# Performance work log

Hardware: AMD Instinct MI355X
Metric: run time of the kernel (lower is better)

## Reference

```python
import jax, jax.numpy as jnp
import numpy as np

TEMP = 0.5
EPS = 1e-8  # torch CosineSimilarity eps


def setup_inputs() -> dict:
    key = jax.random.key(0)
    k1, k2 = jax.random.split(key)
    B, D = 4096, 512
    z_i = jax.random.normal(k1, (B, D), dtype=jnp.float32)
    z_j = jax.random.normal(k2, (B, D), dtype=jnp.float32)
    return {"z_i": z_i, "z_j": z_j}


def reference(z_i, z_j):
    B = z_i.shape[0]
    N = 2 * B
    z = jnp.concatenate([z_i, z_j], axis=0)              # [N, D]
    norm = jnp.maximum(jnp.linalg.norm(z, axis=1, keepdims=True), EPS)
    zn = z / norm                                        # unit rows
    sim = jnp.matmul(zn, zn.T) / TEMP                    # [N, N] cosine sims / temperature
    # positives: sim[i, i+B] for i<B and sim[i+B, i] for i<B
    pos = jnp.concatenate([jnp.diagonal(sim, offset=B), jnp.diagonal(sim, offset=-B)])  # [N]
    # CE over logits [pos, negatives] with label 0 == -pos + logsumexp(row without diagonal)
    diag_mask = jnp.eye(N, dtype=bool)
    sim_masked = jnp.where(diag_mask, -jnp.inf, sim)
    lse = jax.nn.logsumexp(sim_masked, axis=1)           # [N]
    loss = jnp.sum(lse - pos) / N                        # CrossEntropyLoss(reduction='sum') / N
    return loss
```

## Files before the change

kernel.cpp:

```cpp
#include <hip/hip_runtime.h>
#include <stdint.h>

#define NROWS 8192
#define HALF_N 4096
#define DIM 512
#define INV_TEMP 2.0f
#define E2SCALE 2.8853900817779268f
#define LN2 0.6931471805599453f
#define NTILES 528
#define NXCD 8
#define TPX (NTILES / NXCD)

typedef int i32x8 __attribute__((ext_vector_type(8)));
typedef float f32x16 __attribute__((ext_vector_type(16)));

__device__ __forceinline__ void gload_lds16(const unsigned char* g, unsigned char* l) {
  __builtin_amdgcn_global_load_lds(
      (const __attribute__((address_space(1))) unsigned int*)(uintptr_t)g,
      (__attribute__((address_space(3))) unsigned int*)(uint32_t)(uintptr_t)l,
      16, 0, 0);
}

__global__ void __launch_bounds__(256) k_normalize(const float* __restrict__ zi,
                                                   const float* __restrict__ zj,
                                                   unsigned char* __restrict__ zn,
                                                   float* __restrict__ sumexp) {
  int tid = threadIdx.x;
  int gid = blockIdx.x * 256 + tid;
  if (gid < NROWS) sumexp[gid] = 0.0f;
  int wave = tid >> 6, lane = tid & 63;
  int row = blockIdx.x * 4 + wave;
  const float* src = (row < HALF_N) ? (zi + (size_t)row * DIM)
                                    : (zj + (size_t)(row - HALF_N) * DIM);
  const float4* s4 = (const float4*)src;
  float4 a = s4[lane];
  float4 b = s4[lane + 64];
  float ss = a.x * a.x + a.y * a.y + a.z * a.z + a.w * a.w +
             b.x * b.x + b.y * b.y + b.z * b.z + b.w * b.w;
#pragma unroll
  for (int off = 32; off > 0; off >>= 1) ss += __shfl_xor(ss, off, 64);
  float inv = 1.0f / fmaxf(sqrtf(ss), 1e-8f);
  int w0 = __builtin_amdgcn_cvt_pk_fp8_f32(a.x * inv, a.y * inv, 0, false);
  w0 = __builtin_amdgcn_cvt_pk_fp8_f32(a.z * inv, a.w * inv, w0, true);
  int w1 = __builtin_amdgcn_cvt_pk_fp8_f32(b.x * inv, b.y * inv, 0, false);
  w1 = __builtin_amdgcn_cvt_pk_fp8_f32(b.z * inv, b.w * inv, w1, true);
  unsigned char* dst = zn + (size_t)row * DIM;
  *((int*)(dst + lane * 4)) = w0;
  *((int*)(dst + 256 + lane * 4)) = w1;
}

__global__ void __launch_bounds__(512, 2) k_simsum(const unsigned char* __restrict__ zn,
                                                   float* __restrict__ sumexp,
                                                   float* __restrict__ posv) {
  __shared__ __align__(16) unsigned char As[3][256 * 64];
  __shared__ __align__(16) unsigned char Bs[3][256 * 64];
  int tid = threadIdx.x;
  int wave = tid >> 6, lane = tid & 63;

  int bswz = (blockIdx.x & (NXCD - 1)) * TPX + (blockIdx.x >> 3);
  int idx = bswz;
  int tn = (int)((sqrtf(8.0f * idx + 1.0f) - 1.0f) * 0.5f);
  while (tn * (tn + 1) / 2 > idx) tn--;
  while ((tn + 1) * (tn + 2) / 2 <= idx) tn++;
  int tm = idx - tn * (tn + 1) / 2;
  int rowBase = tm * 256, colBase = tn * 256;
  int wr = (wave >> 2) * 128, wc = (wave & 3) * 64;
  int h = lane >> 5, c32 = lane & 31;

  int rA = wave * 32 + (lane >> 2);
  int chunk = (lane & 3) ^ ((rA >> 1) & 3);
  const unsigned char* gA = zn + (size_t)(rowBase + rA) * DIM + chunk * 16;
  const unsigned char* gB = zn + (size_t)(colBase + rA) * DIM + chunk * 16;

#define STAGE(b)                                            \
  do {                                                      \
    gload_lds16(gA, &As[b][wave * 2048]);                   \
    gload_lds16(gA + 16 * DIM, &As[b][wave * 2048 + 1024]); \
    gload_lds16(gB, &Bs[b][wave * 2048]);                   \
    gload_lds16(gB + 16 * DIM, &Bs[b][wave * 2048 + 1024]); \
    gA += 64; gB += 64;                                     \
  } while (0)

  f32x16 acc[4][2];
#pragma unroll
  for (int i = 0; i < 4; i++)
#pragma unroll
    for (int j = 0; j < 2; j++)
#pragma unroll
      for (int r = 0; r < 16; r++) acc[i][j][r] = 0.f;

  int sg = (c32 >> 1) & 3;
  int p0 = (2 * h) ^ sg, p1 = p0 ^ 1;
  int aIdx[4] = {(wr + c32) * 4, (wr + 32 + c32) * 4,
                 (wr + 64 + c32) * 4, (wr + 96 + c32) * 4};
  int bIdx[2] = {(wc + c32) * 4, (wc + 32 + c32) * 4};

#define COMPUTE(b)                                                                   \
  do {                                                                               \
    const int4* Av = (const int4*)As[b];                                             \
    const int4* Bv = (const int4*)Bs[b];                                             \
    i32x8 af[4], bfr[2];                                                             \
    _Pragma("unroll") for (int i = 0; i < 4; i++) {                                  \
      int4 lo = Av[aIdx[i] + p0], hi = Av[aIdx[i] + p1];                             \
      af[i] = (i32x8){lo.x, lo.y, lo.z, lo.w, hi.x, hi.y, hi.z, hi.w};               \
    }                                                                                \
    _Pragma("unroll") for (int j = 0; j < 2; j++) {                                  \
      int4 lo = Bv[bIdx[j] + p0], hi = Bv[bIdx[j] + p1];                             \
      bfr[j] = (i32x8){lo.x, lo.y, lo.z, lo.w, hi.x, hi.y, hi.z, hi.w};              \
    }                                                                                \
    __builtin_amdgcn_s_setprio(1);                                                   \
    _Pragma("unroll") for (int i = 0; i < 4; i++)                                    \
      _Pragma("unroll") for (int j = 0; j < 2; j++)                                  \
        acc[i][j] = __builtin_amdgcn_mfma_scale_f32_32x32x64_f8f6f4(                 \
            af[i], bfr[j], acc[i][j], 0, 0,                               \
            0, 0x7F, 0, 0x7F);                                     \
    __builtin_amdgcn_s_setprio(0);                                                   \
  } while (0)

#define ASM_VMCNT(n) asm volatile("s_waitcnt vmcnt(" #n ")" ::: "memory")
#define WINDOW(s, vm)                                        \
  do {                                                       \
    ASM_VMCNT(vm);                                           \
    asm volatile("s_waitcnt lgkmcnt(0)" ::: "memory");       \
    __builtin_amdgcn_sched_barrier(0);                       \
    __builtin_amdgcn_s_barrier();                            \
    __builtin_amdgcn_sched_barrier(0);                       \
    if ((s) + 2 < 8) STAGE(((s) + 2) % 3);                   \
    COMPUTE((s) % 3);                                        \
  } while (0)

  STAGE(0);
  STAGE(1);
  WINDOW(0, 4);
  WINDOW(1, 4);
  WINDOW(2, 4);
  WINDOW(3, 4);
  WINDOW(4, 4);
  WINDOW(5, 4);
  WINDOW(6, 4);
  WINDOW(7, 0);

  bool isDiag = (tm == tn);
  bool hasPos = (tn == tm + 16);
  bool diagLane = (h == ((c32 >> 2) & 1));
  int rsel = (c32 & 3) | ((c32 >> 3) << 2);
  int dj = 2 * (wave & 3) - 4 * (wave >> 2);

  if (diagLane) {
    if (isDiag) {
      if (dj == 0) { acc[0][0][rsel] = -1e30f; acc[1][1][rsel] = -1e30f; }
      else if (dj == 2) { acc[2][0][rsel] = -1e30f; acc[3][1][rsel] = -1e30f; }
    }
    if (hasPos) {
      if (dj == 0) {
        int gr = rowBase + wr + c32;
        float s0 = acc[0][0][rsel] * INV_TEMP, s1 = acc[1][1][rsel] * INV_TEMP;
        posv[gr] = s0; posv[gr + HALF_N] = s0;
        posv[gr + 32] = s1; posv[gr + 32 + HALF_N] = s1;
      } else if (dj == 2) {
        int gr = rowBase + wr + 64 + c32;
        float s0 = acc[2][0][rsel] * INV_TEMP, s1 = acc[3][1][rsel] * INV_TEMP;
        posv[gr] = s0; posv[gr + HALF_N] = s0;
        posv[gr + 32] = s1; posv[gr + 32 + HALF_N] = s1;
      }
    }
  }

  float cp[2] = {0.f, 0.f};
#pragma unroll
  for (int i = 0; i < 4; i++)
#pragma unroll
    for (int r = 0; r < 16; r++) {
      float e0 = __builtin_amdgcn_exp2f(acc[i][0][r] * E2SCALE);
      float e1 = __builtin_amdgcn_exp2f(acc[i][1][r] * E2SCALE);
      cp[0] += e0;
      cp[1] += e1;
      acc[i][0][r] = e0 + e1;
    }

#define FOLD5(RPX)                                                 \
  do {                                                             \
    _Pragma("unroll") for (int t = 0; t < 16; t++) {               \
      float mine = (lane & 16) ? RPX(t + 16) : RPX(t);             \
      float oth = __shfl_xor((lane & 16) ? RPX(t) : RPX(t + 16), 16, 64); \
      RPX(t) = mine + oth;                                         \
    }                                                              \
    _Pragma("unroll") for (int t = 0; t < 8; t++) {                \
      float mine = (lane & 8) ? RPX(t + 8) : RPX(t);               \
      float oth = __shfl_xor((lane & 8) ? RPX(t) : RPX(t + 8), 8, 64); \
      RPX(t) = mine + oth;                                         \
    }                                                              \
    _Pragma("unroll") for (int t = 0; t < 4; t++) {                \
      float mine = (lane & 4) ? RPX(t + 4) : RPX(t);               \
      float oth = __shfl_xor((lane & 4) ? RPX(t) : RPX(t + 4), 4, 64); \
      RPX(t) = mine + oth;                                         \
    }                                                              \
    _Pragma("unroll") for (int t = 0; t < 2; t++) {                \
      float mine = (lane & 2) ? RPX(t + 2) : RPX(t);               \
      float oth = __shfl_xor((lane & 2) ? RPX(t) : RPX(t + 2), 2, 64); \
      RPX(t) = mine + oth;                                         \
    }                                                              \
    {                                                              \
      float mine = (lane & 1) ? RPX(1) : RPX(0);                   \
      float oth = __shfl_xor((lane & 1) ? RPX(0) : RPX(1), 1, 64); \
      RPX(0) = mine + oth;                                         \
    }                                                              \
  } while (0)

#define RPA(t) acc[(t) >> 4][0][(t) & 15]
#define RPB(t) acc[2 + ((t) >> 4)][0][(t) & 15]
  int myrow = rowBase + wr + 32 * (c32 >> 4) + (c32 & 3) + 8 * ((c32 >> 2) & 3) + 4 * h;
  FOLD5(RPA);
  atomicAdd(&sumexp[myrow], RPA(0));
  FOLD5(RPB);
  atomicAdd(&sumexp[myrow + 64], RPB(0));
#undef RPA
#undef RPB

  if (!isDiag) {
    cp[0] += __shfl_xor(cp[0], 32, 64);
    cp[1] += __shfl_xor(cp[1], 32, 64);
    float cv = h ? cp[1] : cp[0];
    atomicAdd(&sumexp[colBase + wc + h * 32 + c32], cv);
  }
#undef STAGE
#undef COMPUTE
#undef WINDOW
#undef ASM_VMCNT
#undef FOLD5
}

__global__ void __launch_bounds__(1024) k_final(const float* __restrict__ sumexp,
                                                const float* __restrict__ posv,
                                                float* __restrict__ out) {
  __shared__ float red[16];
  int tid = threadIdx.x;
  const float4* se4 = (const float4*)sumexp;
  const float4* pv4 = (const float4*)posv;
  float p = 0.f;
#pragma unroll
  for (int c = 0; c < 2; c++) {
    float4 se = se4[tid * 2 + c];
    float4 pv = pv4[tid * 2 + c];
    p += (__builtin_amdgcn_logf(se.x) + __builtin_amdgcn_logf(se.y) +
          __builtin_amdgcn_logf(se.z) + __builtin_amdgcn_logf(se.w)) * LN2 -
         (pv.x + pv.y + pv.z + pv.w);
  }
#pragma unroll
  for (int off = 32; off > 0; off >>= 1) p += __shfl_xor(p, off, 64);
  int wv = tid >> 6, ln = tid & 63;
  if (ln == 0) red[wv] = p;
  __syncthreads();
  if (tid == 0) {
    float t = 0.f;
    for (int w = 0; w < 16; w++) t += red[w];
    out[0] = t / (float)NROWS;
  }
}

extern "C" void kernel_launch(void* const* d_in, const int* in_sizes, int n_in,
                              void* d_out, int out_size, void* d_ws, size_t ws_size,
                              hipStream_t stream) {
  const float* zi = (const float*)d_in[0];
  const float* zj = (const float*)d_in[1];
  unsigned char* zn = (unsigned char*)d_ws;
  float* sumexp = (float*)((char*)d_ws + (size_t)NROWS * DIM);
  float* posv = sumexp + NROWS;
  float* out = (float*)d_out;

  hipLaunchKernelGGL(k_normalize, dim3(2048), dim3(256), 0, stream, zi, zj, zn, sumexp);
  hipLaunchKernelGGL(k_simsum, dim3(NTILES), dim3(512), 0, stream, zn, sumexp, posv);
  hipLaunchKernelGGL(k_final, dim3(1), dim3(1024), 0, stream, sumexp, posv, out);
}
```

Before: 98.09 us.

## Use 256x128 rectangular tiles over the upper triangle with per-element masking

```diff
diff --git a/kernel.cpp b/kernel.cpp
--- a/kernel.cpp
+++ b/kernel.cpp
@@ -7,7 +7,7 @@
 #define INV_TEMP 2.0f
 #define E2SCALE 2.8853900817779268f
 #define LN2 0.6931471805599453f
-#define NTILES 528
+#define NTILES 1056
 #define NXCD 8
 #define TPX (NTILES / NXCD)
 
@@ -49,36 +49,43 @@
   *((int*)(dst + 256 + lane * 4)) = w1;
 }
 
-__global__ void __launch_bounds__(512, 2) k_simsum(const unsigned char* __restrict__ zn,
+__global__ void __launch_bounds__(256, 2) k_simsum(const unsigned char* __restrict__ zn,
                                                    float* __restrict__ sumexp,
                                                    float* __restrict__ posv) {
   __shared__ __align__(16) unsigned char As[3][256 * 64];
-  __shared__ __align__(16) unsigned char Bs[3][256 * 64];
+  __shared__ __align__(16) unsigned char Bs[3][128 * 64];
   int tid = threadIdx.x;
   int wave = tid >> 6, lane = tid & 63;
 
-  int bswz = (blockIdx.x & (NXCD - 1)) * TPX + (blockIdx.x >> 3);
-  int idx = bswz;
-  int tn = (int)((sqrtf(8.0f * idx + 1.0f) - 1.0f) * 0.5f);
-  while (tn * (tn + 1) / 2 > idx) tn--;
-  while ((tn + 1) * (tn + 2) / 2 <= idx) tn++;
-  int tm = idx - tn * (tn + 1) / 2;
-  int rowBase = tm * 256, colBase = tn * 256;
-  int wr = (wave >> 2) * 128, wc = (wave & 3) * 64;
+  int b = blockIdx.x;
+  int idx = (b & (NXCD - 1)) * TPX + (b >> 3);
+  int tm = (int)((65.0f - sqrtf(4225.0f - 4.0f * idx)) * 0.5f);
+  while (tm * (65 - tm) > idx) tm--;
+  while ((tm + 1) * (64 - tm) <= idx) tm++;
+  int tn = idx - tm * (63 - tm);
+  int rowBase = tm * 256, colBase = tn * 128;
+
+  int wr = (wave >> 1) * 128, wc = (wave & 1) * 64;
   int h = lane >> 5, c32 = lane & 31;
 
-  int rA = wave * 32 + (lane >> 2);
-  int chunk = (lane & 3) ^ ((rA >> 1) & 3);
-  const unsigned char* gA = zn + (size_t)(rowBase + rA) * DIM + chunk * 16;
-  const unsigned char* gB = zn + (size_t)(colBase + rA) * DIM + chunk * 16;
-
-#define STAGE(b)                                            \
-  do {                                                      \
-    gload_lds16(gA, &As[b][wave * 2048]);                   \
-    gload_lds16(gA + 16 * DIM, &As[b][wave * 2048 + 1024]); \
-    gload_lds16(gB, &Bs[b][wave * 2048]);                   \
-    gload_lds16(gB + 16 * DIM, &Bs[b][wave * 2048 + 1024]); \
-    gA += 64; gB += 64;                                     \
+  int rA = wave * 64 + (lane >> 2);
+  int cA = (lane & 3) ^ ((rA >> 1) & 3);
+  const unsigned char* gA = zn + (size_t)(rowBase + rA) * DIM + cA * 16;
+  int rB = wave * 32 + (lane >> 2);
+  int cB = (lane & 3) ^ ((rB >> 1) & 3);
+  const unsigned char* gB = zn + (size_t)(colBase + rB) * DIM + cB * 16;
+
+#define STAGE(bf)                                     \
+  do {                                                \
+    unsigned char* la = &As[bf][wave * 4096];         \
+    unsigned char* lb = &Bs[bf][wave * 2048];         \
+    gload_lds16(gA, la);                              \
+    gload_lds16(gA + 16 * DIM, la + 1024);            \
+    gload_lds16(gA + 32 * DIM, la + 2048);            \
+    gload_lds16(gA + 48 * DIM, la + 3072);            \
+    gload_lds16(gB, lb);                              \
+    gload_lds16(gB + 16 * DIM, lb + 1024);            \
+    gA += 64; gB += 64;                               \
   } while (0)
 
   f32x16 acc[4][2];
@@ -95,10 +102,10 @@
                  (wr + 64 + c32) * 4, (wr + 96 + c32) * 4};
   int bIdx[2] = {(wc + c32) * 4, (wc + 32 + c32) * 4};
 
-#define COMPUTE(b)                                                                   \
+#define COMPUTE(bf)                                                                  \
   do {                                                                               \
-    const int4* Av = (const int4*)As[b];                                             \
-    const int4* Bv = (const int4*)Bs[b];                                             \
+    const int4* Av = (const int4*)As[bf];                                            \
+    const int4* Bv = (const int4*)Bs[bf];                                            \
     i32x8 af[4], bfr[2];                                                             \
     _Pragma("unroll") for (int i = 0; i < 4; i++) {                                  \
       int4 lo = Av[aIdx[i] + p0], hi = Av[aIdx[i] + p1];                             \
@@ -131,52 +138,51 @@
 
   STAGE(0);
   STAGE(1);
-  WINDOW(0, 4);
-  WINDOW(1, 4);
-  WINDOW(2, 4);
-  WINDOW(3, 4);
-  WINDOW(4, 4);
-  WINDOW(5, 4);
-  WINDOW(6, 4);
+  WINDOW(0, 6);
+  WINDOW(1, 6);
+  WINDOW(2, 6);
+  WINDOW(3, 6);
+  WINDOW(4, 6);
+  WINDOW(5, 6);
+  WINDOW(6, 6);
   WINDOW(7, 0);
 
-  bool isDiag = (tm == tn);
-  bool hasPos = (tn == tm + 16);
+  int dbase = colBase + wc - rowBase - wr;
+  int rsel = (c32 & 3) | ((c32 >> 3) << 2);
   bool diagLane = (h == ((c32 >> 2) & 1));
-  int rsel = (c32 & 3) | ((c32 >> 3) << 2);
-  int dj = 2 * (wave & 3) - 4 * (wave >> 2);
-
-  if (diagLane) {
-    if (isDiag) {
-      if (dj == 0) { acc[0][0][rsel] = -1e30f; acc[1][1][rsel] = -1e30f; }
-      else if (dj == 2) { acc[2][0][rsel] = -1e30f; acc[3][1][rsel] = -1e30f; }
-    }
-    if (hasPos) {
-      if (dj == 0) {
-        int gr = rowBase + wr + c32;
-        float s0 = acc[0][0][rsel] * INV_TEMP, s1 = acc[1][1][rsel] * INV_TEMP;
-        posv[gr] = s0; posv[gr + HALF_N] = s0;
-        posv[gr + 32] = s1; posv[gr + 32 + HALF_N] = s1;
-      } else if (dj == 2) {
-        int gr = rowBase + wr + 64 + c32;
-        float s0 = acc[2][0][rsel] * INV_TEMP, s1 = acc[3][1][rsel] * INV_TEMP;
-        posv[gr] = s0; posv[gr + HALF_N] = s0;
-        posv[gr + 32] = s1; posv[gr + 32 + HALF_N] = s1;
+
+#pragma unroll
+  for (int i = 0; i < 4; i++)
+#pragma unroll
+    for (int j = 0; j < 2; j++) {
+      int d = dbase + j * 32 - i * 32;
+      if (d == HALF_N && diagLane) {
+        float sv = acc[i][j][rsel] * INV_TEMP;
+        int gr = rowBase + wr + i * 32 + c32;
+        posv[gr] = sv;
+        posv[gr + HALF_N] = sv;
       }
     }
-  }
 
   float cp[2] = {0.f, 0.f};
 #pragma unroll
-  for (int i = 0; i < 4; i++)
+  for (int i = 0; i < 4; i++) {
+    int d0 = dbase - i * 32;
+    int d1 = d0 + 32;
 #pragma unroll
     for (int r = 0; r < 16; r++) {
+      int rowIn = (r & 3) + 8 * (r >> 2) + 4 * h;
       float e0 = __builtin_amdgcn_exp2f(acc[i][0][r] * E2SCALE);
       float e1 = __builtin_amdgcn_exp2f(acc[i][1][r] * E2SCALE);
+      bool k0 = (d0 > 0) || ((d0 == 0) && (rowIn < c32));
+      bool k1 = (d1 > 0) || ((d1 == 0) && (rowIn < c32));
+      e0 = k0 ? e0 : 0.f;
+      e1 = k1 ? e1 : 0.f;
       cp[0] += e0;
       cp[1] += e1;
       acc[i][0][r] = e0 + e1;
     }
+  }
 
 #define FOLD5(RPX)                                                 \
   do {                                                             \
@@ -217,12 +223,10 @@
 #undef RPA
 #undef RPB
 
-  if (!isDiag) {
-    cp[0] += __shfl_xor(cp[0], 32, 64);
-    cp[1] += __shfl_xor(cp[1], 32, 64);
-    float cv = h ? cp[1] : cp[0];
-    atomicAdd(&sumexp[colBase + wc + h * 32 + c32], cv);
-  }
+  cp[0] += __shfl_xor(cp[0], 32, 64);
+  cp[1] += __shfl_xor(cp[1], 32, 64);
+  float cv = h ? cp[1] : cp[0];
+  atomicAdd(&sumexp[colBase + wc + h * 32 + c32], cv);
 #undef STAGE
 #undef COMPUTE
 #undef WINDOW
@@ -269,6 +273,6 @@
   float* out = (float*)d_out;
 
   hipLaunchKernelGGL(k_normalize, dim3(2048), dim3(256), 0, stream, zi, zj, zn, sumexp);
-  hipLaunchKernelGGL(k_simsum, dim3(NTILES), dim3(512), 0, stream, zn, sumexp, posv);
+  hipLaunchKernelGGL(k_simsum, dim3(NTILES), dim3(256), 0, stream, zn, sumexp, posv);
   hipLaunchKernelGGL(k_final, dim3(1), dim3(1024), 0, stream, sumexp, posv, out);
 }
```

Measured after the change: 97.15 us. About the same (-1.0%).

## Split each K-step into two barrier-synchronized phases interleaving LDS reads with global prefetch

Applied to the files above, without the earlier changes.

```diff
diff --git a/kernel.cpp b/kernel.cpp
--- a/kernel.cpp
+++ b/kernel.cpp
@@ -72,14 +72,21 @@
   const unsigned char* gA = zn + (size_t)(rowBase + rA) * DIM + chunk * 16;
   const unsigned char* gB = zn + (size_t)(colBase + rA) * DIM + chunk * 16;
 
-#define STAGE(b)                                            \
+#define STAGE_A(bf)                                         \
   do {                                                      \
-    gload_lds16(gA, &As[b][wave * 2048]);                   \
-    gload_lds16(gA + 16 * DIM, &As[b][wave * 2048 + 1024]); \
-    gload_lds16(gB, &Bs[b][wave * 2048]);                   \
-    gload_lds16(gB + 16 * DIM, &Bs[b][wave * 2048 + 1024]); \
-    gA += 64; gB += 64;                                     \
-  } while (0)
+    unsigned char* la = &As[bf][wave * 2048];               \
+    gload_lds16(gA, la);                                    \
+    gload_lds16(gA + 16 * DIM, la + 1024);                  \
+    gA += 64;                                               \
+  } while (0)
+#define STAGE_B(bf)                                         \
+  do {                                                      \
+    unsigned char* lb = &Bs[bf][wave * 2048];               \
+    gload_lds16(gB, lb);                                    \
+    gload_lds16(gB + 16 * DIM, lb + 1024);                  \
+    gB += 64;                                               \
+  } while (0)
+#define NOP ((void)0)
 
   f32x16 acc[4][2];
 #pragma unroll
@@ -95,50 +102,76 @@
                  (wr + 64 + c32) * 4, (wr + 96 + c32) * 4};
   int bIdx[2] = {(wc + c32) * 4, (wc + 32 + c32) * 4};
 
-#define COMPUTE(b)                                                                   \
-  do {                                                                               \
-    const int4* Av = (const int4*)As[b];                                             \
-    const int4* Bv = (const int4*)Bs[b];                                             \
-    i32x8 af[4], bfr[2];                                                             \
-    _Pragma("unroll") for (int i = 0; i < 4; i++) {                                  \
-      int4 lo = Av[aIdx[i] + p0], hi = Av[aIdx[i] + p1];                             \
-      af[i] = (i32x8){lo.x, lo.y, lo.z, lo.w, hi.x, hi.y, hi.z, hi.w};               \
-    }                                                                                \
-    _Pragma("unroll") for (int j = 0; j < 2; j++) {                                  \
-      int4 lo = Bv[bIdx[j] + p0], hi = Bv[bIdx[j] + p1];                             \
-      bfr[j] = (i32x8){lo.x, lo.y, lo.z, lo.w, hi.x, hi.y, hi.z, hi.w};              \
-    }                                                                                \
-    __builtin_amdgcn_s_setprio(1);                                                   \
-    _Pragma("unroll") for (int i = 0; i < 4; i++)                                    \
-      _Pragma("unroll") for (int j = 0; j < 2; j++)                                  \
-        acc[i][j] = __builtin_amdgcn_mfma_scale_f32_32x32x64_f8f6f4(                 \
-            af[i], bfr[j], acc[i][j], 0, 0,                               \
-            0, 0x7F, 0, 0x7F);                                     \
-    __builtin_amdgcn_s_setprio(0);                                                   \
-  } while (0)
-
+#define PACK8(lo, hi) ((i32x8){lo.x, lo.y, lo.z, lo.w, hi.x, hi.y, hi.z, hi.w})
+#define MF(a, b, c)                                                       \
+  __builtin_amdgcn_mfma_scale_f32_32x32x64_f8f6f4((a), (b), (c), 0, 0,    \
+                                                  0, 0x7F, 0, 0x7F)
 #define ASM_VMCNT(n) asm volatile("s_waitcnt vmcnt(" #n ")" ::: "memory")
-#define WINDOW(s, vm)                                        \
-  do {                                                       \
-    ASM_VMCNT(vm);                                           \
-    asm volatile("s_waitcnt lgkmcnt(0)" ::: "memory");       \
-    __builtin_amdgcn_sched_barrier(0);                       \
-    __builtin_amdgcn_s_barrier();                            \
-    __builtin_amdgcn_sched_barrier(0);                       \
-    if ((s) + 2 < 8) STAGE(((s) + 2) % 3);                   \
-    COMPUTE((s) % 3);                                        \
-  } while (0)
-
-  STAGE(0);
-  STAGE(1);
-  WINDOW(0, 4);
-  WINDOW(1, 4);
-  WINDOW(2, 4);
-  WINDOW(3, 4);
-  WINDOW(4, 4);
-  WINDOW(5, 4);
-  WINDOW(6, 4);
-  WINDOW(7, 0);
+
+  i32x8 bf0, bf1;
+
+#define PHASE1(BC, SA_STMT)                                              \
+  do {                                                                   \
+    const int4* Av = (const int4*)As[BC];                                \
+    const int4* Bv = (const int4*)Bs[BC];                                \
+    int4 a0l = Av[aIdx[0] + p0], a0h = Av[aIdx[0] + p1];                 \
+    int4 a1l = Av[aIdx[1] + p0], a1h = Av[aIdx[1] + p1];                 \
+    int4 b0l = Bv[bIdx[0] + p0], b0h = Bv[bIdx[0] + p1];                 \
+    int4 b1l = Bv[bIdx[1] + p0], b1h = Bv[bIdx[1] + p1];                 \
+    SA_STMT;                                                             \
+    __builtin_amdgcn_sched_barrier(0);                                   \
+    __builtin_amdgcn_s_barrier();                                        \
+    asm volatile("s_waitcnt lgkmcnt(0)" ::: "memory");                   \
+    __builtin_amdgcn_sched_barrier(0);                                   \
+    i32x8 af0 = PACK8(a0l, a0h), af1 = PACK8(a1l, a1h);                  \
+    bf0 = PACK8(b0l, b0h);                                               \
+    bf1 = PACK8(b1l, b1h);                                               \
+    __builtin_amdgcn_s_setprio(1);                                       \
+    acc[0][0] = MF(af0, bf0, acc[0][0]);                                 \
+    acc[0][1] = MF(af0, bf1, acc[0][1]);                                 \
+    acc[1][0] = MF(af1, bf0, acc[1][0]);                                 \
+    acc[1][1] = MF(af1, bf1, acc[1][1]);                                 \
+    __builtin_amdgcn_s_setprio(0);                                       \
+    __builtin_amdgcn_sched_barrier(0);                                   \
+    __builtin_amdgcn_s_barrier();                                        \
+  } while (0)
+
+#define PHASE2(BC, SB_STMT, TAIL_STMT)                                   \
+  do {                                                                   \
+    const int4* Av = (const int4*)As[BC];                                \
+    int4 a2l = Av[aIdx[2] + p0], a2h = Av[aIdx[2] + p1];                 \
+    int4 a3l = Av[aIdx[3] + p0], a3h = Av[aIdx[3] + p1];                 \
+    SB_STMT;                                                             \
+    __builtin_amdgcn_sched_barrier(0);                                   \
+    __builtin_amdgcn_s_barrier();                                        \
+    asm volatile("s_waitcnt lgkmcnt(0)" ::: "memory");                   \
+    __builtin_amdgcn_sched_barrier(0);                                   \
+    i32x8 af2 = PACK8(a2l, a2h), af3 = PACK8(a3l, a3h);                  \
+    __builtin_amdgcn_s_setprio(1);                                       \
+    acc[2][0] = MF(af2, bf0, acc[2][0]);                                 \
+    acc[2][1] = MF(af2, bf1, acc[2][1]);                                 \
+    acc[3][0] = MF(af3, bf0, acc[3][0]);                                 \
+    acc[3][1] = MF(af3, bf1, acc[3][1]);                                 \
+    __builtin_amdgcn_s_setprio(0);                                       \
+    TAIL_STMT;                                                           \
+    __builtin_amdgcn_sched_barrier(0);                                   \
+    __builtin_amdgcn_s_barrier();                                        \
+  } while (0)
+
+  STAGE_A(0); STAGE_B(0);
+  STAGE_A(1); STAGE_B(1);
+  ASM_VMCNT(4);
+  __builtin_amdgcn_sched_barrier(0);
+  __builtin_amdgcn_s_barrier();
+
+  PHASE1(0, STAGE_A(2)); PHASE2(0, STAGE_B(2), ASM_VMCNT(4));
+  PHASE1(1, STAGE_A(0)); PHASE2(1, STAGE_B(0), ASM_VMCNT(4));
+  PHASE1(2, STAGE_A(1)); PHASE2(2, STAGE_B(1), ASM_VMCNT(4));
+  PHASE1(0, STAGE_A(2)); PHASE2(0, STAGE_B(2), ASM_VMCNT(4));
+  PHASE1(1, STAGE_A(0)); PHASE2(1, STAGE_B(0), ASM_VMCNT(4));
+  PHASE1(2, STAGE_A(1)); PHASE2(2, STAGE_B(1), ASM_VMCNT(4));
+  PHASE1(0, NOP);        PHASE2(0, NOP,        ASM_VMCNT(0));
+  PHASE1(1, NOP);        PHASE2(1, NOP,        NOP);
 
   bool isDiag = (tm == tn);
   bool hasPos = (tn == tm + 16);
@@ -223,10 +256,14 @@
     float cv = h ? cp[1] : cp[0];
     atomicAdd(&sumexp[colBase + wc + h * 32 + c32], cv);
   }
-#undef STAGE
-#undef COMPUTE
-#undef WINDOW
+#undef STAGE_A
+#undef STAGE_B
+#undef NOP
+#undef PACK8
+#undef MF
 #undef ASM_VMCNT
+#undef PHASE1
+#undef PHASE2
 #undef FOLD5
 }
 
```

Result: no change. 99.91 us (+1.9%).
